# Optimization experiments

Hardware: AMD Instinct MI355X
Metric: run time of the kernel (lower is better)

The kernel has to match this reference:

```python
import jax, jax.numpy as jnp
import numpy as np

D_IN, D_K, D_V, BLOCK = 1024, 64, 64, 2048
B, T = 4, 2048

def setup_inputs() -> dict:
    key = jax.random.key(0)
    k0, k1, k2, k3 = jax.random.split(key, 4)
    x = jax.random.normal(k0, (B, T, D_IN), dtype=jnp.float32)
    s = 1.0 / np.sqrt(D_IN)
    Wq = jax.random.normal(k1, (D_IN, D_K), dtype=jnp.float32) * s
    Wk = jax.random.normal(k2, (D_IN, D_K), dtype=jnp.float32) * s
    Wv = jax.random.normal(k3, (D_IN, D_V), dtype=jnp.float32) * s
    return {"x": x, "Wq": Wq, "Wk": Wk, "Wv": Wv}

def reference(x, Wq, Wk, Wv):
    # Q,K,V projections (Linear without bias)
    Q = jnp.einsum('btc,ck->btk', x, Wq)
    K = jnp.einsum('btc,ck->btk', x, Wk)
    V = jnp.einsum('btc,cv->btv', x, Wv)
    Tq = x.shape[1]
    scores = jnp.einsum('bqk,btk->bqt', Q, K)  # [B,T,T]
    causal = jnp.tril(jnp.ones((Tq, Tq), dtype=bool))
    scores = jnp.where(causal, scores, -jnp.inf)
    attn = jax.nn.softmax(scores, axis=-1)
    # NOTE: original divides the AV product by sqrt(d_k) AFTER softmax
    out = jnp.einsum('bqt,btv->bqv', attn, V) / jnp.sqrt(jnp.asarray(K.shape[-1], dtype=x.dtype))
    return out
```

## Files before the change

kernel.cpp:

```cpp
#include <hip/hip_runtime.h>
#include <math.h>

typedef unsigned short u16;
typedef unsigned int uint32;
typedef __attribute__((ext_vector_type(4))) float f32x4;
typedef __attribute__((ext_vector_type(4))) unsigned int u32x4;
typedef __bf16 bf16x8 __attribute__((ext_vector_type(8)));

#define MFMA16(a,b,c) __builtin_amdgcn_mfma_f32_16x16x32_bf16((a),(b),(c),0,0,0)

typedef const __attribute__((address_space(1))) unsigned GU;
typedef __attribute__((address_space(3))) unsigned LU;
__device__ __forceinline__ void gl_lds16(const void* g, void* l) {
    __builtin_amdgcn_global_load_lds((GU*)g, (LU*)l, 16, 0, 0);
}

__device__ __forceinline__ u16 f2b(float f) {
    __bf16 h = (__bf16)f;
    return __builtin_bit_cast(u16, h);
}
__device__ __forceinline__ float b2f(u16 u) {
    unsigned v = (unsigned)u << 16;
    return __builtin_bit_cast(float, v);
}

__device__ __forceinline__ void agload4(f32x4& d, const float* p) {
    asm volatile("global_load_dwordx4 %0, %1, off" : "=&v"(d) : "v"(p) : "memory");
}
__device__ __forceinline__ void dsr(bf16x8& d, uint32 a) {
    u32x4 tmp;
    asm volatile("ds_read_b128 %0, %1" : "=&v"(tmp) : "v"(a) : "memory");
    d = __builtin_bit_cast(bf16x8, tmp);
}
#define WAITVM_I(n) asm volatile("s_waitcnt vmcnt(" #n ")" ::: "memory")
#define WAITVM(n) WAITVM_I(n)

__global__ __launch_bounds__(128) void wtrans_kernel(
    const float* __restrict__ Wq, const float* __restrict__ Wk,
    const float* __restrict__ Wv, u16* __restrict__ Wt2)
{
    const int n = blockIdx.x;
    const float* W = (n < 64) ? Wq : ((n < 128) ? Wk : Wv);
    const int nc = n & 63, cg = n >> 4, r = n & 15;
    const int t = threadIdx.x;
    const int k0 = t * 8;
    const int kstep = k0 >> 6, kh = (k0 >> 5) & 1, kg = (k0 >> 3) & 3;
    u16 hh[8], ll[8];
#pragma unroll
    for (int i = 0; i < 8; ++i) {
        const float a = W[(size_t)(k0 + i) * 64 + nc];
        hh[i] = f2b(a);
        ll[i] = f2b(a - b2f(hh[i]));
    }
    const size_t fi = (((size_t)kstep * 12 + cg) * 2 + kh) * 2;
    u16* dst = Wt2 + fi * 512 + kg * 128 + r * 8;
    uint4 vh, vl;
    vh.x = (uint)hh[0] | ((uint)hh[1] << 16); vh.y = (uint)hh[2] | ((uint)hh[3] << 16);
    vh.z = (uint)hh[4] | ((uint)hh[5] << 16); vh.w = (uint)hh[6] | ((uint)hh[7] << 16);
    vl.x = (uint)ll[0] | ((uint)ll[1] << 16); vl.y = (uint)ll[2] | ((uint)ll[3] << 16);
    vl.z = (uint)ll[4] | ((uint)ll[5] << 16); vl.w = (uint)ll[6] | ((uint)ll[7] << 16);
    *(uint4*)dst         = vh;
    *(uint4*)(dst + 512) = vl;
}

__device__ __forceinline__ void stage6(const u16* __restrict__ Wt2,
                                       u16 (&WB)[4][3][6][512],
                                       int w, int nq, int reg, int step, int kh, int lane) {
#pragma unroll
    for (int i = 0; i < 3; ++i)
#pragma unroll
        for (int hl = 0; hl < 2; ++hl) {
            const int fi = ((step * 12 + nq * 3 + i) * 2 + kh) * 2 + hl;
            gl_lds16(Wt2 + (size_t)fi * 512 + lane * 8, &WB[w][reg][i * 2 + hl][0]);
        }
}
__device__ __forceinline__ void issue8(f32x4 (&xs)[8], const float* r0, const float* r1, int step) {
#pragma unroll
    for (int kh = 0; kh < 2; ++kh)
#pragma unroll
        for (int j = 0; j < 2; ++j) {
            agload4(xs[0 * 4 + kh * 2 + j], r0 + step * 64 + kh * 32 + j * 4);
            agload4(xs[1 * 4 + kh * 2 + j], r1 + step * 64 + kh * 32 + j * 4);
        }
}
__device__ __forceinline__ void conv8(bf16x8& ah, bf16x8& al, f32x4 a, f32x4 b) {
#pragma unroll
    for (int e = 0; e < 4; ++e) {
        { float v = a[e]; __bf16 hb = (__bf16)v; ah[e] = hb; al[e] = (__bf16)(v - (float)hb); }
        { float v = b[e]; __bf16 hb = (__bf16)v; ah[4 + e] = hb; al[4 + e] = (__bf16)(v - (float)hb); }
    }
}

#define PROJ_HALF(H_, WC_)                                                          \
    do {                                                                            \
        if ((H_) + 2 <= 31) {                                                       \
            stage6(Wt2, WB, w, nq, ((H_) + 2) % 3, ((H_) + 2) >> 1, ((H_) + 2) & 1, lane); \
        }                                                                           \
        if ((((H_) & 1) == 0) && ((H_) >> 1) + 2 <= 15) {                           \
            issue8(xr[(((H_) >> 1) + 2) % 3], xrow0, xrow1, ((H_) >> 1) + 2);       \
        }                                                                           \
        WAITVM(WC_);                                                                \
        __builtin_amdgcn_sched_barrier(0);                                          \
        bf16x8 wh0, wl0, wh1, wl1, wh2, wl2;                                        \
        dsr(wh0, dsa + (uint32)((((H_) % 3) * 6 + 0) * 1024));                      \
        dsr(wl0, dsa + (uint32)((((H_) % 3) * 6 + 1) * 1024));                      \
        dsr(wh1, dsa + (uint32)((((H_) % 3) * 6 + 2) * 1024));                      \
        dsr(wl1, dsa + (uint32)((((H_) % 3) * 6 + 3) * 1024));                      \
        dsr(wh2, dsa + (uint32)((((H_) % 3) * 6 + 4) * 1024));                      \
        dsr(wl2, dsa + (uint32)((((H_) % 3) * 6 + 5) * 1024));                      \
        asm volatile("s_waitcnt lgkmcnt(0)" ::: "memory");                          \
        __builtin_amdgcn_sched_barrier(0);                                          \
        _Pragma("unroll")                                                           \
        for (int rg = 0; rg < 2; ++rg) {                                            \
            bf16x8 ah, al;                                                          \
            conv8(ah, al, xr[((H_) >> 1) % 3][rg * 4 + ((H_) & 1) * 2 + 0],         \
                          xr[((H_) >> 1) % 3][rg * 4 + ((H_) & 1) * 2 + 1]);        \
            acc[rg][0] = MFMA16(ah, wh0, acc[rg][0]);                               \
            acc[rg][0] = MFMA16(ah, wl0, acc[rg][0]);                               \
            acc[rg][0] = MFMA16(al, wh0, acc[rg][0]);                               \
            acc[rg][1] = MFMA16(ah, wh1, acc[rg][1]);                               \
            acc[rg][1] = MFMA16(ah, wl1, acc[rg][1]);                               \
            acc[rg][1] = MFMA16(al, wh1, acc[rg][1]);                               \
            acc[rg][2] = MFMA16(ah, wh2, acc[rg][2]);                               \
            acc[rg][2] = MFMA16(ah, wl2, acc[rg][2]);                               \
            acc[rg][2] = MFMA16(al, wh2, acc[rg][2]);                               \
        }                                                                           \
    } while (0)

__global__ __launch_bounds__(256) void proj_kernel(
    const float* __restrict__ x, const u16* __restrict__ Wt2,
    u16* __restrict__ Qhi, u16* __restrict__ Qlo,
    u16* __restrict__ Khi, u16* __restrict__ Klo, u16* __restrict__ Vt)
{
    __shared__ u16 WB[4][3][6][512];
    __shared__ u16 vs[32][72];

    const int t = threadIdx.x, w = t >> 6, lane = t & 63;
    const int lo = lane & 15, hi = lane >> 4;
    const int nq = w;
    const int row0 = blockIdx.x * 32;

    f32x4 acc[2][3];
#pragma unroll
    for (int rg = 0; rg < 2; ++rg)
#pragma unroll
        for (int i = 0; i < 3; ++i) acc[rg][i] = (f32x4){0.f, 0.f, 0.f, 0.f};

    const float* xrow0 = x + (size_t)(row0 + lo) * 1024 + hi * 8;
    const float* xrow1 = x + (size_t)(row0 + 16 + lo) * 1024 + hi * 8;
    const uint32 wbase = (uint32)(size_t)(LU*)(&WB[w][0][0][0]);
    const uint32 dsa = wbase + (uint32)lane * 16u;

    f32x4 xr[3][8];

    stage6(Wt2, WB, w, nq, 0, 0, 0, lane);
    issue8(xr[0], xrow0, xrow1, 0);
    stage6(Wt2, WB, w, nq, 1, 0, 1, lane);
    issue8(xr[1], xrow0, xrow1, 1);

    PROJ_HALF(0, 28);  PROJ_HALF(1, 20);  PROJ_HALF(2, 28);  PROJ_HALF(3, 20);
    PROJ_HALF(4, 28);  PROJ_HALF(5, 20);  PROJ_HALF(6, 28);  PROJ_HALF(7, 20);
    PROJ_HALF(8, 28);  PROJ_HALF(9, 20);  PROJ_HALF(10, 28); PROJ_HALF(11, 20);
    PROJ_HALF(12, 28); PROJ_HALF(13, 20); PROJ_HALF(14, 28); PROJ_HALF(15, 20);
    PROJ_HALF(16, 28); PROJ_HALF(17, 20); PROJ_HALF(18, 28); PROJ_HALF(19, 20);
    PROJ_HALF(20, 28); PROJ_HALF(21, 20); PROJ_HALF(22, 28); PROJ_HALF(23, 20);
    PROJ_HALF(24, 28); PROJ_HALF(25, 20); PROJ_HALF(26, 28); PROJ_HALF(27, 20);
    PROJ_HALF(28, 20); PROJ_HALF(29, 12); PROJ_HALF(30, 6);  PROJ_HALF(31, 0);

#pragma unroll
    for (int rg = 0; rg < 2; ++rg)
#pragma unroll
    for (int i = 0; i < 3; ++i) {
        const int cg = nq * 3 + i;
#pragma unroll
        for (int r = 0; r < 4; ++r) {
            const float v = acc[rg][i][r];
            const int row = row0 + rg * 16 + hi * 4 + r;
            const u16 h = f2b(v);
            if (cg < 4) {
                Qhi[(size_t)row * 64 + cg * 16 + lo] = h;
                Qlo[(size_t)row * 64 + cg * 16 + lo] = f2b(v - b2f(h));
            } else if (cg < 8) {
                Khi[(size_t)row * 64 + (cg - 4) * 16 + lo] = h;
                Klo[(size_t)row * 64 + (cg - 4) * 16 + lo] = f2b(v - b2f(h));
            } else {
                vs[rg * 16 + hi * 4 + r][(cg - 8) * 16 + lo] = h;
            }
        }
    }
    __syncthreads();
    {
        const int bb = row0 >> 11, tok0 = row0 & 2047;
        const int d = t >> 2, part = t & 3;
        u16 tmp[8];
#pragma unroll
        for (int i = 0; i < 8; ++i) tmp[i] = vs[part * 8 + i][d];
        uint4 v4;
        v4.x = (uint)tmp[0] | ((uint)tmp[1] << 16);
        v4.y = (uint)tmp[2] | ((uint)tmp[3] << 16);
        v4.z = (uint)tmp[4] | ((uint)tmp[5] << 16);
        v4.w = (uint)tmp[6] | ((uint)tmp[7] << 16);
        *(uint4*)(Vt + (size_t)bb * 131072 + (size_t)d * 2048 + tok0 + part * 8) = v4;
    }
}

__global__ __launch_bounds__(512, 2) void attn_kernel(
    const u16* __restrict__ Qhi, const u16* __restrict__ Qlo,
    const u16* __restrict__ Khi, const u16* __restrict__ Klo,
    const u16* __restrict__ Vt, float* __restrict__ out)
{
    __shared__ u16 P[8][16 * 64];
    __shared__ float OA[8][16][64];
    __shared__ float LS[8][16];

    const int pi = blockIdx.x, b = blockIdx.y;
    const int t = threadIdx.x, w = t >> 6, l = t & 63;
    const int lo = l & 15, hi = l >> 4;

    const u16* Qh = Qhi + (size_t)b * 131072;
    const u16* Ql = Qlo + (size_t)b * 131072;
    const u16* Kh = Khi + (size_t)b * 131072;
    const u16* Kl = Klo + (size_t)b * 131072;
    const u16* V  = Vt  + (size_t)b * 131072;

    u16* Pw = P[w];

#pragma unroll 1
    for (int phase = 0; phase < 2; ++phase) {
        const int p = phase ? pi : (127 - pi);
        const int q0 = p * 16;
        const int nt = (p >> 2) + 1;

        bf16x8 aqh[2], aql[2];
#pragma unroll
        for (int s = 0; s < 2; ++s) {
            aqh[s] = *(const bf16x8*)(Qh + (size_t)(q0 + lo) * 64 + s * 32 + hi * 8);
            aql[s] = *(const bf16x8*)(Ql + (size_t)(q0 + lo) * 64 + s * 32 + hi * 8);
        }

        f32x4 acc[4];
        float ls[4];
#pragma unroll
        for (int r = 0; r < 4; ++r) { acc[r] = (f32x4){0.f,0.f,0.f,0.f}; ls[r] = 0.f; }

        bf16x8 kh[4][2], kl[4][2];
        auto loadK = [&](int j0) {
#pragma unroll
            for (int kg = 0; kg < 4; ++kg)
#pragma unroll
                for (int s = 0; s < 2; ++s) {
                    const size_t off = (size_t)(j0 + kg * 16 + lo) * 64 + s * 32 + hi * 8;
                    kh[kg][s] = *(const bf16x8*)(Kh + off);
                    kl[kg][s] = *(const bf16x8*)(Kl + off);
                }
        };

        if (w < nt) loadK(w * 64);
#pragma unroll 1
        for (int j = w; j < nt; j += 8) {
            const int j0 = j * 64;
            bf16x8 bv[4][2];
#pragma unroll
            for (int dg = 0; dg < 4; ++dg)
#pragma unroll
                for (int s = 0; s < 2; ++s)
                    bv[dg][s] = *(const bf16x8*)(V + (size_t)(dg * 16 + lo) * 2048 + j0 + s * 32 + hi * 8);

            f32x4 S[4];
            const f32x4 zf = (f32x4){0.f,0.f,0.f,0.f};
#pragma unroll
            for (int kg = 0; kg < 4; ++kg) {
                f32x4 sv = zf;
                sv = MFMA16(aqh[0], kh[kg][0], sv);
                sv = MFMA16(aqh[1], kh[kg][1], sv);
                sv = MFMA16(aqh[0], kl[kg][0], sv);
                sv = MFMA16(aqh[1], kl[kg][1], sv);
                sv = MFMA16(aql[0], kh[kg][0], sv);
                sv = MFMA16(aql[1], kh[kg][1], sv);
                S[kg] = sv;
            }

            if (j + 8 < nt) loadK((j + 8) * 64);

            const bool dm = (j == nt - 1);
#pragma unroll
            for (int r = 0; r < 4; ++r) {
                const int row = q0 + hi * 4 + r;
                float sv0 = S[0][r], sv1 = S[1][r], sv2 = S[2][r], sv3 = S[3][r];
                if (dm) {
                    sv0 = (j0 +      lo > row) ? -INFINITY : sv0;
                    sv1 = (j0 + 16 + lo > row) ? -INFINITY : sv1;
                    sv2 = (j0 + 32 + lo > row) ? -INFINITY : sv2;
                    sv3 = (j0 + 48 + lo > row) ? -INFINITY : sv3;
                }
                const u16 u0 = f2b(__expf(sv0)), u1 = f2b(__expf(sv1));
                const u16 u2 = f2b(__expf(sv2)), u3 = f2b(__expf(sv3));
                float ps = b2f(u0) + b2f(u1) + b2f(u2) + b2f(u3);
#pragma unroll
                for (int msk = 8; msk; msk >>= 1) ps += __shfl_xor(ps, msk, 64);
                ls[r] += ps;
                const int rowL = hi * 4 + r;
                const int base = rowL * 64;
                const int sw = rowL & 7;
                Pw[base + (((0 + (lo >> 3)) ^ sw) << 3) + (lo & 7)] = u0;
                Pw[base + (((2 + (lo >> 3)) ^ sw) << 3) + (lo & 7)] = u1;
                Pw[base + (((4 + (lo >> 3)) ^ sw) << 3) + (lo & 7)] = u2;
                Pw[base + (((6 + (lo >> 3)) ^ sw) << 3) + (lo & 7)] = u3;
            }
            const bf16x8 pa0 = *(const bf16x8*)&Pw[lo * 64 + (((hi    ) ^ (lo & 7)) << 3)];
            const bf16x8 pa1 = *(const bf16x8*)&Pw[lo * 64 + (((hi + 4) ^ (lo & 7)) << 3)];
#pragma unroll
            for (int dg = 0; dg < 4; ++dg) {
                acc[dg] = MFMA16(pa0, bv[dg][0], acc[dg]);
                acc[dg] = MFMA16(pa1, bv[dg][1], acc[dg]);
            }
        }

#pragma unroll
        for (int r = 0; r < 4; ++r) {
            if (lo == 0) LS[w][hi * 4 + r] = ls[r];
#pragma unroll
            for (int dg = 0; dg < 4; ++dg) OA[w][hi * 4 + r][dg * 16 + lo] = acc[dg][r];
        }
        __syncthreads();

        {
            const int row = t >> 5, c0 = (t & 31) * 2;
            float s0 = 0.f, s1 = 0.f, Lt = 0.f;
#pragma unroll
            for (int wv = 0; wv < 8; ++wv) {
                s0 += OA[wv][row][c0];
                s1 += OA[wv][row][c0 + 1];
                Lt += LS[wv][row];
            }
            const float inv = 0.125f / Lt;
            float2 o = make_float2(s0 * inv, s1 * inv);
            *(float2*)(out + ((size_t)b * 2048 + q0 + row) * 64 + c0) = o;
        }
        __syncthreads();
    }
}

extern "C" void kernel_launch(void* const* d_in, const int* in_sizes, int n_in,
                              void* d_out, int out_size, void* d_ws, size_t ws_size,
                              hipStream_t stream) {
    const float* x  = (const float*)d_in[0];
    const float* Wq = (const float*)d_in[1];
    const float* Wk = (const float*)d_in[2];
    const float* Wv = (const float*)d_in[3];
    float* outp = (float*)d_out;

    u16* Wt2 = (u16*)d_ws;
    u16* Qhi = Wt2 + 393216;
    u16* Qlo = Qhi + 524288;
    u16* Khi = Qlo + 524288;
    u16* Klo = Khi + 524288;
    u16* Vt  = Klo + 524288;

    wtrans_kernel<<<dim3(192), dim3(128), 0, stream>>>(Wq, Wk, Wv, Wt2);
    proj_kernel<<<dim3(256), dim3(256), 0, stream>>>(x, Wt2, Qhi, Qlo, Khi, Klo, Vt);
    attn_kernel<<<dim3(64, 4), dim3(512), 0, stream>>>(Qhi, Qlo, Khi, Klo, Vt, outp);
}
```

Measured before the change: 63.04 us.

## Halve projection rows per block and double attention waves per block

The projection kernel now handles 16 rows per block instead of 32, launching 512 blocks so more CUs are busy, at the cost of loading each weight tile twice as often. The attention kernel goes from 8 to 16 waves per block, splitting the key tiles across more waves to shorten each wave's serial loop, with larger shared buffers and a 16-way reduction at the end. The vm wait counts are retuned to match the smaller loads. The risks are more weight traffic in the projection, lower occupancy from 1024-thread blocks, and larger reduction overhead in attention.

```diff
diff --git a/kernel.cpp b/kernel.cpp
--- a/kernel.cpp
+++ b/kernel.cpp
@@ -65,23 +65,21 @@
 
 __device__ __forceinline__ void stage6(const u16* __restrict__ Wt2,
                                        u16 (&WB)[4][3][6][512],
-                                       int w, int nq, int reg, int step, int kh, int lane) {
+                                       int w, int reg, int step, int kh, int lane) {
 #pragma unroll
     for (int i = 0; i < 3; ++i)
 #pragma unroll
         for (int hl = 0; hl < 2; ++hl) {
-            const int fi = ((step * 12 + nq * 3 + i) * 2 + kh) * 2 + hl;
+            const int fi = ((step * 12 + w * 3 + i) * 2 + kh) * 2 + hl;
             gl_lds16(Wt2 + (size_t)fi * 512 + lane * 8, &WB[w][reg][i * 2 + hl][0]);
         }
 }
-__device__ __forceinline__ void issue8(f32x4 (&xs)[8], const float* r0, const float* r1, int step) {
+__device__ __forceinline__ void issue4(f32x4 (&xs)[4], const float* r0, int step) {
 #pragma unroll
     for (int kh = 0; kh < 2; ++kh)
 #pragma unroll
-        for (int j = 0; j < 2; ++j) {
-            agload4(xs[0 * 4 + kh * 2 + j], r0 + step * 64 + kh * 32 + j * 4);
-            agload4(xs[1 * 4 + kh * 2 + j], r1 + step * 64 + kh * 32 + j * 4);
-        }
+        for (int j = 0; j < 2; ++j)
+            agload4(xs[kh * 2 + j], r0 + step * 64 + kh * 32 + j * 4);
 }
 __device__ __forceinline__ void conv8(bf16x8& ah, bf16x8& al, f32x4 a, f32x4 b) {
 #pragma unroll
@@ -94,10 +92,10 @@
 #define PROJ_HALF(H_, WC_)                                                          \
     do {                                                                            \
         if ((H_) + 2 <= 31) {                                                       \
-            stage6(Wt2, WB, w, nq, ((H_) + 2) % 3, ((H_) + 2) >> 1, ((H_) + 2) & 1, lane); \
+            stage6(Wt2, WB, w, ((H_) + 2) % 3, ((H_) + 2) >> 1, ((H_) + 2) & 1, lane); \
         }                                                                           \
         if ((((H_) & 1) == 0) && ((H_) >> 1) + 2 <= 15) {                           \
-            issue8(xr[(((H_) >> 1) + 2) % 3], xrow0, xrow1, ((H_) >> 1) + 2);       \
+            issue4(xr[(((H_) >> 1) + 2) % 3], xrow0, ((H_) >> 1) + 2);              \
         }                                                                           \
         WAITVM(WC_);                                                                \
         __builtin_amdgcn_sched_barrier(0);                                          \
@@ -110,20 +108,19 @@
         dsr(wl2, dsa + (uint32)((((H_) % 3) * 6 + 5) * 1024));                      \
         asm volatile("s_waitcnt lgkmcnt(0)" ::: "memory");                          \
         __builtin_amdgcn_sched_barrier(0);                                          \
-        _Pragma("unroll")                                                           \
-        for (int rg = 0; rg < 2; ++rg) {                                            \
+        {                                                                           \
             bf16x8 ah, al;                                                          \
-            conv8(ah, al, xr[((H_) >> 1) % 3][rg * 4 + ((H_) & 1) * 2 + 0],         \
-                          xr[((H_) >> 1) % 3][rg * 4 + ((H_) & 1) * 2 + 1]);        \
-            acc[rg][0] = MFMA16(ah, wh0, acc[rg][0]);                               \
-            acc[rg][0] = MFMA16(ah, wl0, acc[rg][0]);                               \
-            acc[rg][0] = MFMA16(al, wh0, acc[rg][0]);                               \
-            acc[rg][1] = MFMA16(ah, wh1, acc[rg][1]);                               \
-            acc[rg][1] = MFMA16(ah, wl1, acc[rg][1]);                               \
-            acc[rg][1] = MFMA16(al, wh1, acc[rg][1]);                               \
-            acc[rg][2] = MFMA16(ah, wh2, acc[rg][2]);                               \
-            acc[rg][2] = MFMA16(ah, wl2, acc[rg][2]);                               \
-            acc[rg][2] = MFMA16(al, wh2, acc[rg][2]);                               \
+            conv8(ah, al, xr[((H_) >> 1) % 3][((H_) & 1) * 2 + 0],                  \
+                          xr[((H_) >> 1) % 3][((H_) & 1) * 2 + 1]);                 \
+            acc[0] = MFMA16(ah, wh0, acc[0]);                                       \
+            acc[0] = MFMA16(ah, wl0, acc[0]);                                       \
+            acc[0] = MFMA16(al, wh0, acc[0]);                                       \
+            acc[1] = MFMA16(ah, wh1, acc[1]);                                       \
+            acc[1] = MFMA16(ah, wl1, acc[1]);                                       \
+            acc[1] = MFMA16(al, wh1, acc[1]);                                       \
+            acc[2] = MFMA16(ah, wh2, acc[2]);                                       \
+            acc[2] = MFMA16(ah, wl2, acc[2]);                                       \
+            acc[2] = MFMA16(al, wh2, acc[2]);                                       \
         }                                                                           \
     } while (0)
 
@@ -133,49 +130,43 @@
     u16* __restrict__ Khi, u16* __restrict__ Klo, u16* __restrict__ Vt)
 {
     __shared__ u16 WB[4][3][6][512];
-    __shared__ u16 vs[32][72];
+    __shared__ u16 vs[16][72];
 
     const int t = threadIdx.x, w = t >> 6, lane = t & 63;
     const int lo = lane & 15, hi = lane >> 4;
-    const int nq = w;
-    const int row0 = blockIdx.x * 32;
-
-    f32x4 acc[2][3];
-#pragma unroll
-    for (int rg = 0; rg < 2; ++rg)
-#pragma unroll
-        for (int i = 0; i < 3; ++i) acc[rg][i] = (f32x4){0.f, 0.f, 0.f, 0.f};
+    const int row0 = blockIdx.x * 16;
+
+    f32x4 acc[3];
+#pragma unroll
+    for (int i = 0; i < 3; ++i) acc[i] = (f32x4){0.f, 0.f, 0.f, 0.f};
 
     const float* xrow0 = x + (size_t)(row0 + lo) * 1024 + hi * 8;
-    const float* xrow1 = x + (size_t)(row0 + 16 + lo) * 1024 + hi * 8;
     const uint32 wbase = (uint32)(size_t)(LU*)(&WB[w][0][0][0]);
     const uint32 dsa = wbase + (uint32)lane * 16u;
 
-    f32x4 xr[3][8];
-
-    stage6(Wt2, WB, w, nq, 0, 0, 0, lane);
-    issue8(xr[0], xrow0, xrow1, 0);
-    stage6(Wt2, WB, w, nq, 1, 0, 1, lane);
-    issue8(xr[1], xrow0, xrow1, 1);
-
-    PROJ_HALF(0, 28);  PROJ_HALF(1, 20);  PROJ_HALF(2, 28);  PROJ_HALF(3, 20);
-    PROJ_HALF(4, 28);  PROJ_HALF(5, 20);  PROJ_HALF(6, 28);  PROJ_HALF(7, 20);
-    PROJ_HALF(8, 28);  PROJ_HALF(9, 20);  PROJ_HALF(10, 28); PROJ_HALF(11, 20);
-    PROJ_HALF(12, 28); PROJ_HALF(13, 20); PROJ_HALF(14, 28); PROJ_HALF(15, 20);
-    PROJ_HALF(16, 28); PROJ_HALF(17, 20); PROJ_HALF(18, 28); PROJ_HALF(19, 20);
-    PROJ_HALF(20, 28); PROJ_HALF(21, 20); PROJ_HALF(22, 28); PROJ_HALF(23, 20);
-    PROJ_HALF(24, 28); PROJ_HALF(25, 20); PROJ_HALF(26, 28); PROJ_HALF(27, 20);
-    PROJ_HALF(28, 20); PROJ_HALF(29, 12); PROJ_HALF(30, 6);  PROJ_HALF(31, 0);
-
-#pragma unroll
-    for (int rg = 0; rg < 2; ++rg)
+    f32x4 xr[3][4];
+
+    stage6(Wt2, WB, w, 0, 0, 0, lane);
+    issue4(xr[0], xrow0, 0);
+    stage6(Wt2, WB, w, 1, 0, 1, lane);
+    issue4(xr[1], xrow0, 1);
+
+    PROJ_HALF(0, 20);  PROJ_HALF(1, 20);  PROJ_HALF(2, 20);  PROJ_HALF(3, 16);
+    PROJ_HALF(4, 20);  PROJ_HALF(5, 16);  PROJ_HALF(6, 20);  PROJ_HALF(7, 16);
+    PROJ_HALF(8, 20);  PROJ_HALF(9, 16);  PROJ_HALF(10, 20); PROJ_HALF(11, 16);
+    PROJ_HALF(12, 20); PROJ_HALF(13, 16); PROJ_HALF(14, 20); PROJ_HALF(15, 16);
+    PROJ_HALF(16, 20); PROJ_HALF(17, 16); PROJ_HALF(18, 20); PROJ_HALF(19, 16);
+    PROJ_HALF(20, 20); PROJ_HALF(21, 16); PROJ_HALF(22, 20); PROJ_HALF(23, 16);
+    PROJ_HALF(24, 20); PROJ_HALF(25, 16); PROJ_HALF(26, 20); PROJ_HALF(27, 16);
+    PROJ_HALF(28, 16); PROJ_HALF(29, 12); PROJ_HALF(30, 6);  PROJ_HALF(31, 0);
+
 #pragma unroll
     for (int i = 0; i < 3; ++i) {
-        const int cg = nq * 3 + i;
+        const int cg = w * 3 + i;
 #pragma unroll
         for (int r = 0; r < 4; ++r) {
-            const float v = acc[rg][i][r];
-            const int row = row0 + rg * 16 + hi * 4 + r;
+            const float v = acc[i][r];
+            const int row = row0 + hi * 4 + r;
             const u16 h = f2b(v);
             if (cg < 4) {
                 Qhi[(size_t)row * 64 + cg * 16 + lo] = h;
@@ -184,7 +175,7 @@
                 Khi[(size_t)row * 64 + (cg - 4) * 16 + lo] = h;
                 Klo[(size_t)row * 64 + (cg - 4) * 16 + lo] = f2b(v - b2f(h));
             } else {
-                vs[rg * 16 + hi * 4 + r][(cg - 8) * 16 + lo] = h;
+                vs[hi * 4 + r][(cg - 8) * 16 + lo] = h;
             }
         }
     }
@@ -192,26 +183,24 @@
     {
         const int bb = row0 >> 11, tok0 = row0 & 2047;
         const int d = t >> 2, part = t & 3;
-        u16 tmp[8];
-#pragma unroll
-        for (int i = 0; i < 8; ++i) tmp[i] = vs[part * 8 + i][d];
-        uint4 v4;
-        v4.x = (uint)tmp[0] | ((uint)tmp[1] << 16);
-        v4.y = (uint)tmp[2] | ((uint)tmp[3] << 16);
-        v4.z = (uint)tmp[4] | ((uint)tmp[5] << 16);
-        v4.w = (uint)tmp[6] | ((uint)tmp[7] << 16);
-        *(uint4*)(Vt + (size_t)bb * 131072 + (size_t)d * 2048 + tok0 + part * 8) = v4;
-    }
-}
-
-__global__ __launch_bounds__(512, 2) void attn_kernel(
+        u16 tmp[4];
+#pragma unroll
+        for (int i = 0; i < 4; ++i) tmp[i] = vs[part * 4 + i][d];
+        uint2 v2;
+        v2.x = (uint)tmp[0] | ((uint)tmp[1] << 16);
+        v2.y = (uint)tmp[2] | ((uint)tmp[3] << 16);
+        *(uint2*)(Vt + (size_t)bb * 131072 + (size_t)d * 2048 + tok0 + part * 4) = v2;
+    }
+}
+
+__global__ __launch_bounds__(1024) void attn_kernel(
     const u16* __restrict__ Qhi, const u16* __restrict__ Qlo,
     const u16* __restrict__ Khi, const u16* __restrict__ Klo,
     const u16* __restrict__ Vt, float* __restrict__ out)
 {
-    __shared__ u16 P[8][16 * 64];
-    __shared__ float OA[8][16][64];
-    __shared__ float LS[8][16];
+    __shared__ u16 P[16][16 * 64];
+    __shared__ float OA[16][16][64];
+    __shared__ float LS[16][16];
 
     const int pi = blockIdx.x, b = blockIdx.y;
     const int t = threadIdx.x, w = t >> 6, l = t & 63;
@@ -257,7 +246,7 @@
 
         if (w < nt) loadK(w * 64);
 #pragma unroll 1
-        for (int j = w; j < nt; j += 8) {
+        for (int j = w; j < nt; j += 16) {
             const int j0 = j * 64;
             bf16x8 bv[4][2];
 #pragma unroll
@@ -280,7 +269,7 @@
                 S[kg] = sv;
             }
 
-            if (j + 8 < nt) loadK((j + 8) * 64);
+            if (j + 16 < nt) loadK((j + 16) * 64);
 
             const bool dm = (j == nt - 1);
 #pragma unroll
@@ -325,17 +314,14 @@
         __syncthreads();
 
         {
-            const int row = t >> 5, c0 = (t & 31) * 2;
-            float s0 = 0.f, s1 = 0.f, Lt = 0.f;
-#pragma unroll
-            for (int wv = 0; wv < 8; ++wv) {
-                s0 += OA[wv][row][c0];
-                s1 += OA[wv][row][c0 + 1];
+            const int row = t >> 6, c = t & 63;
+            float s0 = 0.f, Lt = 0.f;
+#pragma unroll
+            for (int wv = 0; wv < 16; ++wv) {
+                s0 += OA[wv][row][c];
                 Lt += LS[wv][row];
             }
-            const float inv = 0.125f / Lt;
-            float2 o = make_float2(s0 * inv, s1 * inv);
-            *(float2*)(out + ((size_t)b * 2048 + q0 + row) * 64 + c0) = o;
+            out[((size_t)b * 2048 + q0 + row) * 64 + c] = s0 * (0.125f / Lt);
         }
         __syncthreads();
     }
@@ -358,6 +344,6 @@
     u16* Vt  = Klo + 524288;
 
     wtrans_kernel<<<dim3(192), dim3(128), 0, stream>>>(Wq, Wk, Wv, Wt2);
-    proj_kernel<<<dim3(256), dim3(256), 0, stream>>>(x, Wt2, Qhi, Qlo, Khi, Klo, Vt);
-    attn_kernel<<<dim3(64, 4), dim3(512), 0, stream>>>(Qhi, Qlo, Khi, Klo, Vt, outp);
-}
+    proj_kernel<<<dim3(512), dim3(256), 0, stream>>>(x, Wt2, Qhi, Qlo, Khi, Klo, Vt);
+    attn_kernel<<<dim3(64, 4), dim3(1024), 0, stream>>>(Qhi, Qlo, Khi, Klo, Vt, outp);
+}
```

Measured after the change: 115.6 us. 1.83x slower.
